# Optimization experiments

Hardware: AMD Instinct MI355X
Metric: run time of the kernel (lower is better)

## Reference

```python
import jax, jax.numpy as jnp
import numpy as np
from jax import lax


def setup_inputs() -> dict:
    key = jax.random.key(0)
    ks = jax.random.split(key, 8)
    B, N, q = 16, 4096, 256
    sc = float(1.0 / np.sqrt(q))
    return {
        "u": jax.random.normal(ks[0], (B, N, q), jnp.float32),
        "a": jax.random.normal(ks[1], (q,), jnp.float32),  # diag of A
        "W_B": jax.random.normal(ks[2], (q, q), jnp.float32) * sc,
        "b_B": jax.random.normal(ks[3], (q,), jnp.float32) * sc,
        "W_C": jax.random.normal(ks[4], (q, q), jnp.float32) * sc,
        "b_C": jax.random.normal(ks[5], (q,), jnp.float32) * sc,
        "W_D": jax.random.normal(ks[6], (q, q), jnp.float32) * sc,
        "b_D": jax.random.normal(ks[7], (q,), jnp.float32) * sc,
    }


def _solve_im(u, a, W_B, b_B, dt):
    """IM solver. A is diagonal, so M_inv is four diagonal blocks:
    new_x = s*x - dt*s*a*z ; new_z = dt*s*x + s*z, with s = 1/(1+dt^2*a).
    Forcing F = M_inv @ [dt*B(u); 0] -> (dt*s*Bu, dt^2*s*Bu)."""
    s = 1.0 / (1.0 + dt * dt * a)  # (q,)
    Bu = jnp.einsum("bnq,pq->bnp", u, W_B) + b_B  # (B,N,q), torch Linear: u @ W^T + b
    f_x = (dt * s) * Bu
    f_z = (dt * dt * s) * Bu
    dsa = dt * s * a
    ds = dt * s

    def step(carry, f):
        x, z = carry
        fx, fz = f
        x_new = s * x - dsa * z + fx
        z_new = ds * x + s * z + fz
        return (x_new, z_new), z_new

    Bsz, _, q = u.shape
    init = (jnp.zeros((Bsz, q), u.dtype), jnp.zeros((Bsz, q), u.dtype))
    # scan over time axis
    _, z_t = lax.scan(step, init, (jnp.moveaxis(f_x, 1, 0), jnp.moveaxis(f_z, 1, 0)))
    return jnp.moveaxis(z_t, 0, 1)  # (B,N,q) -- the out[..., size:] half


def reference(u, a, W_B, b_B, W_C, b_C, W_D, b_D):
    N = u.shape[1]
    dt = 1.0 / N
    y = _solve_im(u, a, W_B, b_B, dt)
    x = (jnp.einsum("bnq,pq->bnp", y, W_C) + b_C) + (jnp.einsum("bnq,pq->bnp", u, W_D) + b_D)
    x = jax.nn.gelu(x, approximate=False)  # torch GELU default = exact erf
    # GLU(concat([x, x], -1)) == x * sigmoid(x)
    out = x * jax.nn.sigmoid(x) + u
    return (out, y)
```

## Files before the change

kernel.cpp:

```cpp
#include <hip/hip_runtime.h>
#include <hip/hip_bf16.h>
#include <cstdint>

typedef __bf16 bf16_t;
typedef __bf16 bf16x8 __attribute__((ext_vector_type(8)));
typedef float f32x4 __attribute__((ext_vector_type(4)));

#define B_SZ 16
#define N_SZ 4096
#define Q_SZ 256
#define M_TOT (B_SZ * N_SZ)
#define DT (1.0f / 4096.0f)
#define LDST 40
#define CHUNKS 64
#define LOG2_CLEN 6
#define CLEN (N_SZ / CHUNKS)
#define TPAD 133


__device__ __forceinline__ bf16x8 load8f(const float* p) {
  const float4 v0 = *(const float4*)p;
  const float4 v1 = *(const float4*)(p + 4);
  bf16x8 v;
  v[0] = (bf16_t)v0.x; v[1] = (bf16_t)v0.y; v[2] = (bf16_t)v0.z; v[3] = (bf16_t)v0.w;
  v[4] = (bf16_t)v1.x; v[5] = (bf16_t)v1.y; v[6] = (bf16_t)v1.z; v[7] = (bf16_t)v1.w;
  return v;
}

__device__ __forceinline__ int pidx(int tm, int tk, int lane) {
  return ((tm * 8 + tk) * 64 + lane) * 8;
}

__device__ __forceinline__ void kpassP(const bf16_t* __restrict__ A,
                                       const bf16_t* __restrict__ Bw,
                                       int tmA, int tnB, int lane,
                                       f32x4 acc[4][4]) {
#pragma unroll
  for (int tk = 0; tk < 8; ++tk) {
    bf16x8 af[4], bv[4];
#pragma unroll
    for (int i = 0; i < 4; ++i) {
      af[i] = *(const bf16x8*)(A + pidx(tmA + i, tk, lane));
      bv[i] = *(const bf16x8*)(Bw + pidx(tnB + i, tk, lane));
    }
#pragma unroll
    for (int mi = 0; mi < 4; ++mi)
#pragma unroll
      for (int ni = 0; ni < 4; ++ni)
        acc[mi][ni] = __builtin_amdgcn_mfma_f32_16x16x32_bf16(af[mi], bv[ni],
                                                              acc[mi][ni], 0, 0, 0);
  }
}

__global__ __launch_bounds__(256) void prep_kernel(
    const float* __restrict__ u, const float* __restrict__ WB,
    const float* __restrict__ WC, const float* __restrict__ WD,
    bf16_t* __restrict__ ubP, bf16_t* __restrict__ WBbP,
    bf16_t* __restrict__ WCbP, bf16_t* __restrict__ WDbP) {
  const int g = blockIdx.x * 256 + threadIdx.x;
  const int UC = (M_TOT * Q_SZ) / 8;
  const float* src;
  bf16_t* dst;
  int cidx;
  if (g < UC) {
    src = u; dst = ubP; cidx = g;
  } else {
    const int h = g - UC;
    const int w = h >> 13;
    cidx = h & 8191;
    src = (w == 0) ? WB : (w == 1) ? WC : WD;
    dst = (w == 0) ? WBbP : (w == 1) ? WCbP : WDbP;
  }
  const int lane = cidx & 63, tk = (cidx >> 6) & 7, tm = cidx >> 9;
  const int row = tm * 16 + (lane & 15);
  const int col = tk * 32 + (lane >> 4) * 8;
  *(bf16x8*)(dst + (size_t)cidx * 8) = load8f(src + (size_t)row * Q_SZ + col);
}

__global__ __launch_bounds__(256, 2) void gemm1f_kernel(
    const bf16_t* __restrict__ ubP, const bf16_t* __restrict__ WBbP,
    const float* __restrict__ a, const float* __restrict__ bB,
    float* __restrict__ ex, float* __restrict__ ez,
    float* __restrict__ lz) {
  __shared__ float T[2][64][TPAD];
  const int t = threadIdx.x;
  const int bid = blockIdx.x;
  const int swz = (bid & 7) * 128 + (bid >> 3);
  const int m0 = (swz >> 1) * 128, n0 = (swz & 1) * 128;
  const int lane = t & 63, ln = lane & 15, quad = lane >> 4;
  const int wave = t >> 6;
  const int wm = (wave & 1) * 64, wn = (wave >> 1) * 64;
  f32x4 acc[4][4] = {};
  kpassP(ubP, WBbP, (m0 + wm) >> 4, (n0 + wn) >> 4, lane, acc);

  const int cc = wave & 1;
#pragma unroll
  for (int ni = 0; ni < 4; ++ni) {
    const int colL = wn + ni * 16 + ln;
    const int gp = n0 + colL;
    const float av = a[gp];
    const float s = 1.0f / (1.0f + DT * DT * av);
    const float sc = DT * s;
    const float bb = bB[gp];
#pragma unroll
    for (int mi = 0; mi < 4; ++mi) {
      const int nrow = mi * 16 + quad * 4;
#pragma unroll
      for (int r2 = 0; r2 < 4; ++r2)
        T[cc][nrow + r2][colL] = sc * (acc[mi][ni][r2] + bb);
    }
  }
  __syncthreads();

  const int scc = t >> 7, col = t & 127;
  const int pg = n0 + col;
  {
    const float av = a[pg];
    const float s = 1.0f / (1.0f + DT * DT * av);
    const float dsa = DT * s * av, dss = DT * s;
    const int mbase = m0 + scc * 64;
    float x = 0.f, z = 0.f;
    float* lp = lz + (size_t)mbase * Q_SZ + pg;
#pragma unroll 8
    for (int n = 0; n < 64; ++n) {
      const float f = T[scc][n][col];
      const float xn = fmaf(s, x, fmaf(-dsa, z, f));
      const float zn = fmaf(dss, x, fmaf(s, z, DT * f));
      x = xn; z = zn;
      lp[(size_t)n * Q_SZ] = zn;
    }
    const int chunk_g = mbase >> 6;
    ex[chunk_g * 256 + pg] = x;
    ez[chunk_g * 256 + pg] = z;
  }
}

__global__ __launch_bounds__(256) void scan2_kernel(
    const float* __restrict__ a, const float* __restrict__ ex,
    const float* __restrict__ ez, float* __restrict__ ix, float* __restrict__ iz) {
  const int g = blockIdx.x * 256 + threadIdx.x;
  const int p = g & 255, b = g >> 8;
  const float av = a[p];
  const float s = 1.0f / (1.0f + DT * DT * av);
  float m00 = s, m01 = -DT * s * av, m10 = DT * s, m11 = s;
#pragma unroll
  for (int i = 0; i < LOG2_CLEN; ++i) {
    const float a00 = fmaf(m00, m00, m01 * m10);
    const float a01 = m01 * (m00 + m11);
    const float a10 = m10 * (m00 + m11);
    const float a11 = fmaf(m11, m11, m01 * m10);
    m00 = a00; m01 = a01; m10 = a10; m11 = a11;
  }
  float x = 0.f, z = 0.f;
  for (int c = 0; c < CHUNKS; ++c) {
    const size_t idx = ((size_t)b * CHUNKS + c) * Q_SZ + p;
    ix[idx] = x; iz[idx] = z;
    const float xn = fmaf(m00, x, fmaf(m01, z, ex[idx]));
    const float zn = fmaf(m10, x, fmaf(m11, z, ez[idx]));
    x = xn; z = zn;
  }
}

__global__ __launch_bounds__(256) void mpow_kernel(
    const float* __restrict__ a, float* __restrict__ t10,
    float* __restrict__ t11) {
  const int p = threadIdx.x;
  const float av = a[p];
  const float s = 1.0f / (1.0f + DT * DT * av);
  const float m00 = s, m01 = -DT * s * av, m10 = DT * s, m11 = s;
  float p00 = m00, p01 = m01, p10 = m10, p11 = m11;
  for (int n = 0; n < 64; ++n) {
    t10[n * 256 + p] = p10;
    t11[n * 256 + p] = p11;
    const float q00 = fmaf(m00, p00, m01 * p10);
    const float q01 = fmaf(m00, p01, m01 * p11);
    const float q10 = fmaf(m10, p00, m11 * p10);
    const float q11 = fmaf(m10, p01, m11 * p11);
    p00 = q00; p01 = q01; p10 = q10; p11 = q11;
  }
}

__global__ __launch_bounds__(256) void fix3_kernel(
    const float* __restrict__ ix, const float* __restrict__ iz,
    const float* __restrict__ t10, const float* __restrict__ t11,
    float* __restrict__ y, bf16_t* __restrict__ ybP) {
  const int g = blockIdx.x * 256 + threadIdx.x;
  const int m = g >> 5, p0 = (g & 31) * 8;
  const int nloc = m & 63, cg = m >> 6;
  float* yp = y + (size_t)m * Q_SZ + p0;
  const f32x4 l0 = *(const f32x4*)yp;
  const f32x4 l1 = *(const f32x4*)(yp + 4);
  const f32x4 tA0 = *(const f32x4*)(t10 + nloc * 256 + p0);
  const f32x4 tA1 = *(const f32x4*)(t10 + nloc * 256 + p0 + 4);
  const f32x4 tB0 = *(const f32x4*)(t11 + nloc * 256 + p0);
  const f32x4 tB1 = *(const f32x4*)(t11 + nloc * 256 + p0 + 4);
  const f32x4 X0 = *(const f32x4*)(ix + cg * 256 + p0);
  const f32x4 X1 = *(const f32x4*)(ix + cg * 256 + p0 + 4);
  const f32x4 Z0 = *(const f32x4*)(iz + cg * 256 + p0);
  const f32x4 Z1 = *(const f32x4*)(iz + cg * 256 + p0 + 4);
  f32x4 y0, y1;
#pragma unroll
  for (int e = 0; e < 4; ++e) {
    y0[e] = fmaf(tA0[e], X0[e], fmaf(tB0[e], Z0[e], l0[e]));
    y1[e] = fmaf(tA1[e], X1[e], fmaf(tB1[e], Z1[e], l1[e]));
  }
  *(f32x4*)yp = y0;
  *(f32x4*)(yp + 4) = y1;
  bf16x8 v;
#pragma unroll
  for (int e = 0; e < 4; ++e) {
    v[e] = (bf16_t)y0[e];
    v[e + 4] = (bf16_t)y1[e];
  }
  const int chunk = ((m >> 4) * 8 + (p0 >> 5)) * 64 +
                    ((((p0 >> 3) & 3) << 4) | (m & 15));
  *(bf16x8*)(ybP + (size_t)chunk * 8) = v;
}

__global__ __launch_bounds__(256, 2) void gemm2p_kernel(
    const bf16_t* __restrict__ ybP, const bf16_t* __restrict__ WCbP,
    const bf16_t* __restrict__ ubP, const bf16_t* __restrict__ WDbP,
    const float* __restrict__ u, const float* __restrict__ bC,
    const float* __restrict__ bD, float* __restrict__ out0) {
  const int t = threadIdx.x;
  const int bid = blockIdx.x;
  const int swz = (bid & 7) * 128 + (bid >> 3);
  const int m0 = (swz >> 1) * 128, n0 = (swz & 1) * 128;
  const int lane = t & 63, ln = lane & 15, quad = lane >> 4;
  const int wave = t >> 6;
  const int wm = (wave & 1) * 64, wn = (wave >> 1) * 64;
  const int tmA = (m0 + wm) >> 4, tnB = (n0 + wn) >> 4;
  f32x4 acc[4][4] = {};
#pragma unroll
  for (int tk = 0; tk < 8; ++tk) {
    bf16x8 a1[4], b1[4], a2[4], b2[4];
#pragma unroll
    for (int i = 0; i < 4; ++i) {
      a1[i] = *(const bf16x8*)(ybP + pidx(tmA + i, tk, lane));
      b1[i] = *(const bf16x8*)(WCbP + pidx(tnB + i, tk, lane));
      a2[i] = *(const bf16x8*)(ubP + pidx(tmA + i, tk, lane));
      b2[i] = *(const bf16x8*)(WDbP + pidx(tnB + i, tk, lane));
    }
#pragma unroll
    for (int mi = 0; mi < 4; ++mi)
#pragma unroll
      for (int ni = 0; ni < 4; ++ni)
        acc[mi][ni] = __builtin_amdgcn_mfma_f32_16x16x32_bf16(a1[mi], b1[ni],
                                                              acc[mi][ni], 0, 0, 0);
#pragma unroll
    for (int mi = 0; mi < 4; ++mi)
#pragma unroll
      for (int ni = 0; ni < 4; ++ni)
        acc[mi][ni] = __builtin_amdgcn_mfma_f32_16x16x32_bf16(a2[mi], b2[ni],
                                                              acc[mi][ni], 0, 0, 0);
  }
#pragma unroll
  for (int ni = 0; ni < 4; ++ni) {
    const int gp = n0 + wn + ni * 16 + ln;
    const float bias = bC[gp] + bD[gp];
#pragma unroll
    for (int mi = 0; mi < 4; ++mi) {
      const int gm = m0 + wm + mi * 16 + quad * 4;
#pragma unroll
      for (int r2 = 0; r2 < 4; ++r2) {
        const float x = acc[mi][ni][r2] + bias;
        const float g = 0.5f * x * (1.0f + erff(x * 0.70710678118654752f));
        const float sg = 1.0f / (1.0f + __expf(-g));
        const float uu = u[(size_t)(gm + r2) * Q_SZ + gp];
        out0[(size_t)(gm + r2) * Q_SZ + gp] = fmaf(g, sg, uu);
      }
    }
  }
}


__device__ __forceinline__ void kloop(const float* __restrict__ Ap,
                                      const float* __restrict__ Bp,
                                      int m0, int n0, int t,
                                      bf16_t* As, bf16_t* Bs, f32x4 acc[4][4]) {
  const int r = t >> 2, cc = t & 3;
  const int lane = t & 63, ln = lane & 15, quad = lane >> 4;
  const int wave = t >> 6;
  const int wm = (wave & 1) * 64, wn = (wave >> 1) * 64;

  for (int k0 = 0; k0 < Q_SZ; k0 += 32) {
#pragma unroll
    for (int i = 0; i < 2; ++i) {
      const int row = r + i * 64;
      const int col = k0 + cc * 8;
      *(bf16x8*)(As + row * LDST + cc * 8) =
          load8f(Ap + (size_t)(m0 + row) * Q_SZ + col);
      *(bf16x8*)(Bs + row * LDST + cc * 8) =
          load8f(Bp + (size_t)(n0 + row) * Q_SZ + col);
    }
    __syncthreads();
    bf16x8 af[4], bv[4];
#pragma unroll
    for (int mi = 0; mi < 4; ++mi) {
      af[mi] = *(const bf16x8*)(As + (wm + mi * 16 + ln) * LDST + quad * 8);
      bv[mi] = *(const bf16x8*)(Bs + (wn + mi * 16 + ln) * LDST + quad * 8);
    }
#pragma unroll
    for (int mi = 0; mi < 4; ++mi)
#pragma unroll
      for (int ni = 0; ni < 4; ++ni)
        acc[mi][ni] = __builtin_amdgcn_mfma_f32_16x16x32_bf16(af[mi], bv[ni],
                                                              acc[mi][ni], 0, 0, 0);
    __syncthreads();
  }
}

__global__ __launch_bounds__(256) void gemm1_kernel(
    const float* __restrict__ u, const float* __restrict__ WB,
    const float* __restrict__ a, const float* __restrict__ bB,
    float* __restrict__ fx) {
  __shared__ __align__(16) bf16_t As[128 * LDST];
  __shared__ __align__(16) bf16_t Bs[128 * LDST];
  const int t = threadIdx.x;
  const int m0 = blockIdx.x * 128, n0 = blockIdx.y * 128;
  f32x4 acc[4][4] = {};
  kloop(u, WB, m0, n0, t, As, Bs, acc);

  const int lane = t & 63, ln = lane & 15, quad = lane >> 4;
  const int wave = t >> 6;
  const int wm = (wave & 1) * 64, wn = (wave >> 1) * 64;
#pragma unroll
  for (int ni = 0; ni < 4; ++ni) {
    const int gp = n0 + wn + ni * 16 + ln;
    const float av = a[gp];
    const float s = 1.0f / (1.0f + DT * DT * av);
    const float sc = DT * s;
    const float bb = bB[gp];
#pragma unroll
    for (int mi = 0; mi < 4; ++mi) {
      const int gm = m0 + wm + mi * 16 + quad * 4;
#pragma unroll
      for (int r2 = 0; r2 < 4; ++r2)
        fx[(size_t)(gm + r2) * Q_SZ + gp] = sc * (acc[mi][ni][r2] + bb);
    }
  }
}

__global__ __launch_bounds__(256) void gemm2_kernel(
    const float* __restrict__ y, const float* __restrict__ WC,
    const float* __restrict__ u, const float* __restrict__ WD,
    const float* __restrict__ bC, const float* __restrict__ bD,
    float* __restrict__ out0) {
  __shared__ __align__(16) bf16_t As[128 * LDST];
  __shared__ __align__(16) bf16_t Bs[128 * LDST];
  const int t = threadIdx.x;
  const int m0 = blockIdx.x * 128, n0 = blockIdx.y * 128;
  f32x4 acc[4][4] = {};
  kloop(y, WC, m0, n0, t, As, Bs, acc);
  kloop(u, WD, m0, n0, t, As, Bs, acc);

  const int lane = t & 63, ln = lane & 15, quad = lane >> 4;
  const int wave = t >> 6;
  const int wm = (wave & 1) * 64, wn = (wave >> 1) * 64;
#pragma unroll
  for (int ni = 0; ni < 4; ++ni) {
    const int gp = n0 + wn + ni * 16 + ln;
    const float bias = bC[gp] + bD[gp];
#pragma unroll
    for (int mi = 0; mi < 4; ++mi) {
      const int gm = m0 + wm + mi * 16 + quad * 4;
#pragma unroll
      for (int r2 = 0; r2 < 4; ++r2) {
        const float x = acc[mi][ni][r2] + bias;
        const float g = 0.5f * x * (1.0f + erff(x * 0.70710678118654752f));
        const float sg = 1.0f / (1.0f + __expf(-g));
        const float uu = u[(size_t)(gm + r2) * Q_SZ + gp];
        out0[(size_t)(gm + r2) * Q_SZ + gp] = fmaf(g, sg, uu);
      }
    }
  }
}

__global__ __launch_bounds__(256) void scan1_kernel(
    const float* __restrict__ fx, const float* __restrict__ a,
    float* __restrict__ ex, float* __restrict__ ez) {
  const int g = blockIdx.x * 256 + threadIdx.x;
  const int p = g & 255, c = (g >> 8) & (CHUNKS - 1), b = g >> 14;
  const float av = a[p];
  const float s = 1.0f / (1.0f + DT * DT * av);
  const float dsa = DT * s * av, dss = DT * s;
  float x = 0.f, z = 0.f;
  const float* fp = fx + ((size_t)b * N_SZ + c * CLEN) * Q_SZ + p;
  for (int n = 0; n < CLEN; ++n) {
    const float f = fp[(size_t)n * Q_SZ];
    const float xn = fmaf(s, x, fmaf(-dsa, z, f));
    const float zn = fmaf(dss, x, fmaf(s, z, DT * f));
    x = xn; z = zn;
  }
  ex[g] = x; ez[g] = z;
}

__global__ __launch_bounds__(256) void scan3_kernel(
    const float* __restrict__ a, const float* __restrict__ ix,
    const float* __restrict__ iz, float* __restrict__ yf) {
  const int g = blockIdx.x * 256 + threadIdx.x;
  const int p = g & 255, c = (g >> 8) & (CHUNKS - 1), b = g >> 14;
  const float av = a[p];
  const float s = 1.0f / (1.0f + DT * DT * av);
  const float dsa = DT * s * av, dss = DT * s;
  float x = ix[g], z = iz[g];
  float* yp = yf + ((size_t)b * N_SZ + c * CLEN) * Q_SZ + p;
  for (int n = 0; n < CLEN; ++n) {
    const float f = yp[(size_t)n * Q_SZ];
    const float xn = fmaf(s, x, fmaf(-dsa, z, f));
    const float zn = fmaf(dss, x, fmaf(s, z, DT * f));
    x = xn; z = zn;
    yp[(size_t)n * Q_SZ] = zn;
  }
}

__global__ __launch_bounds__(256) void scan_mono_kernel(
    const float* __restrict__ a, float* __restrict__ yf) {
  const int g = blockIdx.x * 256 + threadIdx.x;
  const int p = g & 255, b = g >> 8;
  const float av = a[p];
  const float s = 1.0f / (1.0f + DT * DT * av);
  const float dsa = DT * s * av, dss = DT * s;
  float x = 0.f, z = 0.f;
  float* yp = yf + (size_t)b * N_SZ * Q_SZ + p;
  for (int n = 0; n < N_SZ; ++n) {
    const float f = yp[(size_t)n * Q_SZ];
    const float xn = fmaf(s, x, fmaf(-dsa, z, f));
    const float zn = fmaf(dss, x, fmaf(s, z, DT * f));
    x = xn; z = zn;
    yp[(size_t)n * Q_SZ] = zn;
  }
}


extern "C" void kernel_launch(void* const* d_in, const int* in_sizes, int n_in,
                              void* d_out, int out_size, void* d_ws, size_t ws_size,
                              hipStream_t stream) {
  const float* u  = (const float*)d_in[0];
  const float* a  = (const float*)d_in[1];
  const float* WB = (const float*)d_in[2];
  const float* bB = (const float*)d_in[3];
  const float* WC = (const float*)d_in[4];
  const float* bC = (const float*)d_in[5];
  const float* WD = (const float*)d_in[6];
  const float* bD = (const float*)d_in[7];

  float* out0 = (float*)d_out;
  float* yreg = out0 + (size_t)M_TOT * Q_SZ;

  const size_t UB_ELEMS = (size_t)M_TOT * Q_SZ;
  const size_t W_ELEMS = (size_t)Q_SZ * Q_SZ;
  const size_t ST_ELEMS = (size_t)B_SZ * CHUNKS * Q_SZ;
  const size_t need_full =
      UB_ELEMS * sizeof(bf16_t) +
      UB_ELEMS * sizeof(bf16_t) +
      3 * W_ELEMS * sizeof(bf16_t) +
      4 * ST_ELEMS * sizeof(float) +
      2 * 64 * 256 * sizeof(float);
  const size_t state_bytes = 4 * ST_ELEMS * sizeof(float);

  if (ws_size >= need_full) {
    bf16_t* ubP  = (bf16_t*)d_ws;
    bf16_t* ybP  = ubP + UB_ELEMS;
    bf16_t* WBbP = ybP + UB_ELEMS;
    bf16_t* WCbP = WBbP + W_ELEMS;
    bf16_t* WDbP = WCbP + W_ELEMS;
    float* ex = (float*)(WDbP + W_ELEMS);
    float* ez = ex + ST_ELEMS;
    float* ix = ez + ST_ELEMS;
    float* iz = ix + ST_ELEMS;
    float* t10 = iz + ST_ELEMS;
    float* t11 = t10 + 64 * 256;

    prep_kernel<<<8288, 256, 0, stream>>>(u, WB, WC, WD, ubP, WBbP, WCbP, WDbP);
    gemm1f_kernel<<<1024, 256, 0, stream>>>(ubP, WBbP, a, bB, ex, ez, yreg);
    scan2_kernel<<<16, 256, 0, stream>>>(a, ex, ez, ix, iz);
    mpow_kernel<<<1, 256, 0, stream>>>(a, t10, t11);
    fix3_kernel<<<8192, 256, 0, stream>>>(ix, iz, t10, t11, yreg, ybP);
    gemm2p_kernel<<<1024, 256, 0, stream>>>(ybP, WCbP, ubP, WDbP, u, bC, bD, out0);
  } else {
    dim3 gg(M_TOT / 128, Q_SZ / 128);
    gemm1_kernel<<<gg, 256, 0, stream>>>(u, WB, a, bB, yreg);
    if (ws_size >= state_bytes) {
      float* ex = (float*)d_ws;
      float* ez = ex + ST_ELEMS;
      float* ix = ez + ST_ELEMS;
      float* iz = ix + ST_ELEMS;
      scan1_kernel<<<1024, 256, 0, stream>>>(yreg, a, ex, ez);
      scan2_kernel<<<16, 256, 0, stream>>>(a, ex, ez, ix, iz);
      scan3_kernel<<<1024, 256, 0, stream>>>(a, ix, iz, yreg);
    } else {
      scan_mono_kernel<<<16, 256, 0, stream>>>(a, yreg);
    }
    gemm2_kernel<<<gg, 256, 0, stream>>>(yreg, WC, u, WD, bC, bD, out0);
  }
}
```

Baseline: 325.0 us.

## Retile GEMMs to 64-row full-width blocks with double-buffered register prefetch

Both GEMM kernels move from 128x128 tiles with a swizzled block order to 64-row tiles covering all 256 output columns, with each wave owning a 64-column slice. Their K loops are rewritten to ping-pong two register fragment sets, so the loads for the next k-step are issued before the MFMAs of the current one. Launch bounds are raised to 3 blocks per CU. The A fragment is now loaded once per block across the full N width, and the scan in gemm1 uses all 256 threads on one 64-row chunk. The extra register sets and the shared tile at 3 blocks per CU may cause spills or cap occupancy.

Result: slower. 358.4 us (+10.3%).

```diff
diff --git a/kernel.cpp b/kernel.cpp
--- a/kernel.cpp
+++ b/kernel.cpp
@@ -15,7 +15,7 @@
 #define CHUNKS 64
 #define LOG2_CLEN 6
 #define CLEN (N_SZ / CHUNKS)
-#define TPAD 133
+#define TROW2 264
 
 
 __device__ __forceinline__ bf16x8 load8f(const float* p) {
@@ -29,27 +29,6 @@
 
 __device__ __forceinline__ int pidx(int tm, int tk, int lane) {
   return ((tm * 8 + tk) * 64 + lane) * 8;
-}
-
-__device__ __forceinline__ void kpassP(const bf16_t* __restrict__ A,
-                                       const bf16_t* __restrict__ Bw,
-                                       int tmA, int tnB, int lane,
-                                       f32x4 acc[4][4]) {
-#pragma unroll
-  for (int tk = 0; tk < 8; ++tk) {
-    bf16x8 af[4], bv[4];
-#pragma unroll
-    for (int i = 0; i < 4; ++i) {
-      af[i] = *(const bf16x8*)(A + pidx(tmA + i, tk, lane));
-      bv[i] = *(const bf16x8*)(Bw + pidx(tnB + i, tk, lane));
-    }
-#pragma unroll
-    for (int mi = 0; mi < 4; ++mi)
-#pragma unroll
-      for (int ni = 0; ni < 4; ++ni)
-        acc[mi][ni] = __builtin_amdgcn_mfma_f32_16x16x32_bf16(af[mi], bv[ni],
-                                                              acc[mi][ni], 0, 0, 0);
-  }
 }
 
 __global__ __launch_bounds__(256) void prep_kernel(
@@ -77,61 +56,87 @@
   *(bf16x8*)(dst + (size_t)cidx * 8) = load8f(src + (size_t)row * Q_SZ + col);
 }
 
-__global__ __launch_bounds__(256, 2) void gemm1f_kernel(
+__global__ __launch_bounds__(256, 3) void gemm1i_kernel(
     const bf16_t* __restrict__ ubP, const bf16_t* __restrict__ WBbP,
     const float* __restrict__ a, const float* __restrict__ bB,
     float* __restrict__ ex, float* __restrict__ ez,
     float* __restrict__ lz) {
-  __shared__ float T[2][64][TPAD];
+  __shared__ float T[64][TROW2];
   const int t = threadIdx.x;
-  const int bid = blockIdx.x;
-  const int swz = (bid & 7) * 128 + (bid >> 3);
-  const int m0 = (swz >> 1) * 128, n0 = (swz & 1) * 128;
+  const int m0 = blockIdx.x * 64;
   const int lane = t & 63, ln = lane & 15, quad = lane >> 4;
   const int wave = t >> 6;
-  const int wm = (wave & 1) * 64, wn = (wave >> 1) * 64;
+  const int wn = wave * 64;
+  const int tmA = m0 >> 4, tnB = wn >> 4;
   f32x4 acc[4][4] = {};
-  kpassP(ubP, WBbP, (m0 + wm) >> 4, (n0 + wn) >> 4, lane, acc);
-
-  const int cc = wave & 1;
+
+  bf16x8 aX[4], bX[4], aY[4], bY[4];
+#define G1_LD(SET_A, SET_B, TK)                                             \
+  {                                                                          \
+    _Pragma("unroll") for (int i = 0; i < 4; ++i) {                          \
+      SET_A[i] = *(const bf16x8*)(ubP + pidx(tmA + i, (TK), lane));          \
+      SET_B[i] = *(const bf16x8*)(WBbP + pidx(tnB + i, (TK), lane));         \
+    }                                                                        \
+  }
+#define G1_MM(SET_A, SET_B)                                                  \
+  {                                                                          \
+    _Pragma("unroll") for (int mi = 0; mi < 4; ++mi)                         \
+        _Pragma("unroll") for (int ni = 0; ni < 4; ++ni) acc[mi][ni] =       \
+            __builtin_amdgcn_mfma_f32_16x16x32_bf16(SET_A[mi], SET_B[ni],    \
+                                                    acc[mi][ni], 0, 0, 0);   \
+  }
+  G1_LD(aX, bX, 0);
+  G1_LD(aY, bY, 1);
+  G1_MM(aX, bX);
+  G1_LD(aX, bX, 2);
+  G1_MM(aY, bY);
+  G1_LD(aY, bY, 3);
+  G1_MM(aX, bX);
+  G1_LD(aX, bX, 4);
+  G1_MM(aY, bY);
+  G1_LD(aY, bY, 5);
+  G1_MM(aX, bX);
+  G1_LD(aX, bX, 6);
+  G1_MM(aY, bY);
+  G1_LD(aY, bY, 7);
+  G1_MM(aX, bX);
+  G1_MM(aY, bY);
+#undef G1_LD
+#undef G1_MM
+
 #pragma unroll
   for (int ni = 0; ni < 4; ++ni) {
     const int colL = wn + ni * 16 + ln;
-    const int gp = n0 + colL;
-    const float av = a[gp];
+    const float av = a[colL];
     const float s = 1.0f / (1.0f + DT * DT * av);
     const float sc = DT * s;
-    const float bb = bB[gp];
+    const float bb = bB[colL];
 #pragma unroll
     for (int mi = 0; mi < 4; ++mi) {
       const int nrow = mi * 16 + quad * 4;
 #pragma unroll
       for (int r2 = 0; r2 < 4; ++r2)
-        T[cc][nrow + r2][colL] = sc * (acc[mi][ni][r2] + bb);
+        T[nrow + r2][colL] = sc * (acc[mi][ni][r2] + bb);
     }
   }
   __syncthreads();
 
-  const int scc = t >> 7, col = t & 127;
-  const int pg = n0 + col;
   {
-    const float av = a[pg];
+    const float av = a[t];
     const float s = 1.0f / (1.0f + DT * DT * av);
     const float dsa = DT * s * av, dss = DT * s;
-    const int mbase = m0 + scc * 64;
     float x = 0.f, z = 0.f;
-    float* lp = lz + (size_t)mbase * Q_SZ + pg;
+    float* lp = lz + (size_t)m0 * Q_SZ + t;
 #pragma unroll 8
     for (int n = 0; n < 64; ++n) {
-      const float f = T[scc][n][col];
+      const float f = T[n][t];
       const float xn = fmaf(s, x, fmaf(-dsa, z, f));
       const float zn = fmaf(dss, x, fmaf(s, z, DT * f));
       x = xn; z = zn;
       lp[(size_t)n * Q_SZ] = zn;
     }
-    const int chunk_g = mbase >> 6;
-    ex[chunk_g * 256 + pg] = x;
-    ez[chunk_g * 256 + pg] = z;
+    ex[blockIdx.x * 256 + t] = x;
+    ez[blockIdx.x * 256 + t] = z;
   }
 }
 
@@ -217,50 +222,78 @@
   *(bf16x8*)(ybP + (size_t)chunk * 8) = v;
 }
 
-__global__ __launch_bounds__(256, 2) void gemm2p_kernel(
+__global__ __launch_bounds__(256, 3) void gemm2s_kernel(
     const bf16_t* __restrict__ ybP, const bf16_t* __restrict__ WCbP,
     const bf16_t* __restrict__ ubP, const bf16_t* __restrict__ WDbP,
     const float* __restrict__ u, const float* __restrict__ bC,
     const float* __restrict__ bD, float* __restrict__ out0) {
   const int t = threadIdx.x;
-  const int bid = blockIdx.x;
-  const int swz = (bid & 7) * 128 + (bid >> 3);
-  const int m0 = (swz >> 1) * 128, n0 = (swz & 1) * 128;
+  const int m0 = blockIdx.x * 64;
   const int lane = t & 63, ln = lane & 15, quad = lane >> 4;
   const int wave = t >> 6;
-  const int wm = (wave & 1) * 64, wn = (wave >> 1) * 64;
-  const int tmA = (m0 + wm) >> 4, tnB = (n0 + wn) >> 4;
+  const int wn = wave * 64;
+  const int tmA = m0 >> 4, tnB = wn >> 4;
   f32x4 acc[4][4] = {};
-#pragma unroll
-  for (int tk = 0; tk < 8; ++tk) {
-    bf16x8 a1[4], b1[4], a2[4], b2[4];
-#pragma unroll
-    for (int i = 0; i < 4; ++i) {
-      a1[i] = *(const bf16x8*)(ybP + pidx(tmA + i, tk, lane));
-      b1[i] = *(const bf16x8*)(WCbP + pidx(tnB + i, tk, lane));
-      a2[i] = *(const bf16x8*)(ubP + pidx(tmA + i, tk, lane));
-      b2[i] = *(const bf16x8*)(WDbP + pidx(tnB + i, tk, lane));
-    }
-#pragma unroll
-    for (int mi = 0; mi < 4; ++mi)
-#pragma unroll
-      for (int ni = 0; ni < 4; ++ni)
-        acc[mi][ni] = __builtin_amdgcn_mfma_f32_16x16x32_bf16(a1[mi], b1[ni],
-                                                              acc[mi][ni], 0, 0, 0);
-#pragma unroll
-    for (int mi = 0; mi < 4; ++mi)
-#pragma unroll
-      for (int ni = 0; ni < 4; ++ni)
-        acc[mi][ni] = __builtin_amdgcn_mfma_f32_16x16x32_bf16(a2[mi], b2[ni],
-                                                              acc[mi][ni], 0, 0, 0);
-  }
+
+  bf16x8 aX[4], bX[4], aY[4], bY[4];
+#define G2_LD(SET_A, SET_B, S)                                               \
+  {                                                                          \
+    const bf16_t* Ap_ = ((S) < 8) ? ybP : ubP;                               \
+    const bf16_t* Bp_ = ((S) < 8) ? WCbP : WDbP;                             \
+    _Pragma("unroll") for (int i = 0; i < 4; ++i) {                          \
+      SET_A[i] = *(const bf16x8*)(Ap_ + pidx(tmA + i, (S) & 7, lane));       \
+      SET_B[i] = *(const bf16x8*)(Bp_ + pidx(tnB + i, (S) & 7, lane));       \
+    }                                                                        \
+  }
+#define G2_MM(SET_A, SET_B)                                                  \
+  {                                                                          \
+    _Pragma("unroll") for (int mi = 0; mi < 4; ++mi)                         \
+        _Pragma("unroll") for (int ni = 0; ni < 4; ++ni) acc[mi][ni] =       \
+            __builtin_amdgcn_mfma_f32_16x16x32_bf16(SET_A[mi], SET_B[ni],    \
+                                                    acc[mi][ni], 0, 0, 0);   \
+  }
+  G2_LD(aX, bX, 0);
+  G2_LD(aY, bY, 1);
+  G2_MM(aX, bX);
+  G2_LD(aX, bX, 2);
+  G2_MM(aY, bY);
+  G2_LD(aY, bY, 3);
+  G2_MM(aX, bX);
+  G2_LD(aX, bX, 4);
+  G2_MM(aY, bY);
+  G2_LD(aY, bY, 5);
+  G2_MM(aX, bX);
+  G2_LD(aX, bX, 6);
+  G2_MM(aY, bY);
+  G2_LD(aY, bY, 7);
+  G2_MM(aX, bX);
+  G2_LD(aX, bX, 8);
+  G2_MM(aY, bY);
+  G2_LD(aY, bY, 9);
+  G2_MM(aX, bX);
+  G2_LD(aX, bX, 10);
+  G2_MM(aY, bY);
+  G2_LD(aY, bY, 11);
+  G2_MM(aX, bX);
+  G2_LD(aX, bX, 12);
+  G2_MM(aY, bY);
+  G2_LD(aY, bY, 13);
+  G2_MM(aX, bX);
+  G2_LD(aX, bX, 14);
+  G2_MM(aY, bY);
+  G2_LD(aY, bY, 15);
+  G2_MM(aX, bX);
+  G2_MM(aY, bY);
+#undef G2_LD
+#undef G2_MM
+
 #pragma unroll
   for (int ni = 0; ni < 4; ++ni) {
-    const int gp = n0 + wn + ni * 16 + ln;
+    const int gp = wn + ni * 16 + ln;
     const float bias = bC[gp] + bD[gp];
 #pragma unroll
     for (int mi = 0; mi < 4; ++mi) {
-      const int gm = m0 + wm + mi * 16 + quad * 4;
+      const int gm = m0 + mi * 16 + quad * 4;
 #pragma unroll
       for (int r2 = 0; r2 < 4; ++r2) {
         const float x = acc[mi][ni][r2] + bias;
@@ -473,11 +506,11 @@
     float* t11 = t10 + 64 * 256;
 
     prep_kernel<<<8288, 256, 0, stream>>>(u, WB, WC, WD, ubP, WBbP, WCbP, WDbP);
-    gemm1f_kernel<<<1024, 256, 0, stream>>>(ubP, WBbP, a, bB, ex, ez, yreg);
+    gemm1i_kernel<<<1024, 256, 0, stream>>>(ubP, WBbP, a, bB, ex, ez, yreg);
     scan2_kernel<<<16, 256, 0, stream>>>(a, ex, ez, ix, iz);
     mpow_kernel<<<1, 256, 0, stream>>>(a, t10, t11);
     fix3_kernel<<<8192, 256, 0, stream>>>(ix, iz, t10, t11, yreg, ybP);
-    gemm2p_kernel<<<1024, 256, 0, stream>>>(ybP, WCbP, ubP, WDbP, u, bC, bD, out0);
+    gemm2s_kernel<<<1024, 256, 0, stream>>>(ybP, WCbP, ubP, WDbP, u, bC, bD, out0);
   } else {
     dim3 gg(M_TOT / 128, Q_SZ / 128);
     gemm1_kernel<<<gg, 256, 0, stream>>>(u, WB, a, bB, yreg);
```
